# Kernel tuning notes

Hardware: AMD Instinct MI355X
Metric: run time of the kernel (lower is better)

The kernel has to match this reference:

```python
import jax, jax.numpy as jnp
import numpy as np

B, C, H, W = 64, 3, 224, 224
PH = PW = 16
GH, GW = H // PH, W // PW
NP = GH * GW                        # 196 patches
E = 512                             # embed_dim == decoder_dim
NH = 8                              # num_heads
PPD = C * PH * PW                   # 768 pixels per patch
MASK_RATIO = 0.75
NUM_MASKED = int(MASK_RATIO * NP)   # 147


def setup_inputs() -> dict:
    key = jax.random.key(0)
    ks = jax.random.split(key, 16)
    s = 0.02
    x = jax.random.normal(ks[0], (B, C, H, W), jnp.float32)
    # per-sample random permutation (torch.rand().argsort() equivalent)
    shuffle_indices = jax.vmap(lambda k: jax.random.permutation(k, NP))(
        jax.random.split(ks[1], B)).astype(jnp.int32)
    return {
        "x": x,
        "shuffle_indices": shuffle_indices,
        "W_pe": jax.random.normal(ks[2], (E, PPD), jnp.float32) * s,
        "b_pe": jnp.zeros((E,), jnp.float32),
        "pos_embed": jax.random.normal(ks[3], (1, NP, E), jnp.float32),
        "enc_W": jax.random.normal(ks[4], (E, E), jnp.float32) * s,
        "enc_b": jnp.zeros((E,), jnp.float32),
        "in_proj_w": jax.random.normal(ks[5], (3 * E, E), jnp.float32) * s,
        "in_proj_b": jnp.zeros((3 * E,), jnp.float32),
        "out_w": jax.random.normal(ks[6], (E, E), jnp.float32) * s,
        "out_b": jnp.zeros((E,), jnp.float32),
        "head_W": jax.random.normal(ks[7], (PPD, E), jnp.float32) * s,
        "head_b": jnp.zeros((PPD,), jnp.float32),
        # torch.randn_like(mask_patches) noise, passed in for determinism
        "noise": jax.random.normal(ks[8], (B, NUM_MASKED, PPD), jnp.float32),
    }


def _to_img(p):
    # [b, nP, ph*pw*c] -> [b, c, H, W] (inverse of patchify)
    return p.reshape(B, GH, GW, PH, PW, C).transpose(0, 5, 1, 3, 2, 4).reshape(B, C, H, W)


def reference(x, shuffle_indices, W_pe, b_pe, pos_embed, enc_W, enc_b,
              in_proj_w, in_proj_b, out_w, out_b, head_W, head_b, noise):
    hd = E // NH
    # patchify: [b,c,H,W] -> [b, nP, ph*pw*c]
    patches = x.reshape(B, C, GH, PH, GW, PW).transpose(0, 2, 4, 3, 5, 1).reshape(B, NP, PPD)

    mask_ind = shuffle_indices[:, :NUM_MASKED]      # [b, 147]
    unmask_ind = shuffle_indices[:, NUM_MASKED:]    # [b, 49]
    bi = jnp.arange(B)[:, None]
    mask_patches = patches[bi, mask_ind]            # [b,147,768]
    unmask_patches = patches[bi, unmask_ind]        # [b, 49,768]

    # mask_image: unmasked patches copied from x, masked patches = 1
    is_masked = jnp.zeros((B, NP), bool).at[bi, mask_ind].set(True)
    mpix = is_masked.reshape(B, 1, GH, 1, GW, 1)
    mpix = jnp.broadcast_to(mpix, (B, C, GH, PH, GW, PW)).reshape(B, C, H, W)
    mask_image = jnp.where(mpix, jnp.ones_like(x), x)

    # encode visible tokens
    pe = pos_embed[0]                               # [nP, E]
    unmask_tokens = unmask_patches @ W_pe.T + b_pe + pe[unmask_ind]
    encoded = jax.nn.gelu(unmask_tokens @ enc_W.T + enc_b)   # encoder.transformer stand-in

    # decode: cross attention (queries = mask tokens, kv = encoded)
    mask_tokens = mask_patches @ W_pe.T + b_pe + pe[mask_ind]
    Wq, Wk, Wv = jnp.split(in_proj_w, 3)
    bq, bk, bv = jnp.split(in_proj_b, 3)
    q = (mask_tokens @ Wq.T + bq).reshape(B, NUM_MASKED, NH, hd)
    k = (encoded @ Wk.T + bk).reshape(B, -1, NH, hd)
    v = (encoded @ Wv.T + bv).reshape(B, -1, NH, hd)
    attn = jax.nn.softmax(jnp.einsum('bqhd,bkhd->bhqk', q, k) / jnp.sqrt(jnp.float32(hd)), axis=-1)
    attn_out = jnp.einsum('bhqk,bkhd->bqhd', attn, v).reshape(B, NUM_MASKED, E) @ out_w.T + out_b

    # scatter encoded + attended tokens back into full sequence
    output_tokens = (jnp.zeros((B, NP, E), x.dtype)
                     .at[bi, unmask_ind].set(encoded)
                     .at[bi, mask_ind].set(attn_out))
    dec_mask_tokens = output_tokens[bi, mask_ind]
    pred = dec_mask_tokens @ head_W.T + head_b      # [b,147,768]

    mse_all_patches = jnp.abs(pred - mask_patches).mean(axis=-1).mean()

    recons_patches = jax.lax.stop_gradient(patches).at[bi, mask_ind].set(pred)
    recons_img = _to_img(recons_patches)

    patches_noisy = patches.at[bi, mask_ind].set(noise)
    patches_to_img = _to_img(patches_noisy)

    return recons_img, patches_to_img, mse_all_patches, mask_image
```

## Files before the change

### kernel.cpp

```cpp
#include <hip/hip_runtime.h>
#include <math.h>

typedef __attribute__((ext_vector_type(8))) __bf16 bf16x8;
typedef __attribute__((ext_vector_type(8))) unsigned short u16x8;
typedef __attribute__((ext_vector_type(4))) float f32x4;

typedef unsigned int as1_u32 __attribute__((address_space(1)));
typedef unsigned int as3_u32 __attribute__((address_space(3)));

__device__ __forceinline__ float bf2f(unsigned short h){
  return __uint_as_float(((unsigned int)h) << 16);
}
__device__ __forceinline__ unsigned short f2bf(float f){
  unsigned int u = __float_as_uint(f);
  unsigned int r = (u + 0x7FFFu + ((u >> 16) & 1u)) >> 16;
  return (unsigned short)r;
}

#if __has_builtin(__builtin_amdgcn_global_load_lds)
#define HAVE_GLOAD_LDS 1
__device__ __forceinline__ void gload16(const void* g, void* l){
  __builtin_amdgcn_global_load_lds((const as1_u32*)(unsigned long long)g,
                                   (as3_u32*)l, 16, 0, 0);
}
#else
#define HAVE_GLOAD_LDS 0
#endif

__global__ __launch_bounds__(256) void prep_all(
    const int* __restrict__ shuf, int* __restrict__ slot, int* __restrict__ invp,
    const float* __restrict__ Wpe, const float* __restrict__ outw,
    unsigned short* __restrict__ WpeT, unsigned short* __restrict__ outwT,
    const float* __restrict__ encW, const float* __restrict__ inW,
    const float* __restrict__ headW, unsigned short* __restrict__ wcat,
    const float* __restrict__ pos, const float* __restrict__ b_pe,
    const float* __restrict__ outb, const float* __restrict__ headb,
    unsigned short* __restrict__ pe2b, float* __restrict__ bh32)
{
  const int bid = blockIdx.x, t = threadIdx.x;
  __shared__ float tile[32][33];
  if (bid < 49){
    const int i = bid*256 + t;
    if (i < 64*196){
      const int b = i / 196, j = i % 196;
      const int p = shuf[b*196 + j];
      slot[b*196 + p] = (j < 147) ? j : -1;
      invp[b*196 + p] = j;
    }
  } else if (bid < 689){
    int b2 = bid - 49;
    const float* src; unsigned short* dst; int R, C, bx, by;
    if (b2 < 384){ src = Wpe;  dst = WpeT;  R = 512; C = 768; bx = b2 % 24; by = b2 / 24; }
    else { b2 -= 384; src = outw; dst = outwT; R = 512; C = 512; bx = b2 % 16; by = b2 / 16; }
    const int tx = t & 31, ty = t >> 5;
    #pragma unroll
    for (int i = 0; i < 4; i++)
      tile[ty + i*8][tx] = src[(size_t)(by*32 + ty + i*8)*C + bx*32 + tx];
    __syncthreads();
    #pragma unroll
    for (int i = 0; i < 4; i++)
      dst[(size_t)(bx*32 + ty + i*8)*R + by*32 + tx] = f2bf(tile[tx][ty + i*8]);
  } else if (bid < 6321){
    const int i = (bid - 689)*256 + t;
    float v;
    if      (i <  262144) v = encW[i];
    else if (i < 1048576) v = inW[i -  262144];
    else                  v = headW[i - 1048576];
    wcat[i] = f2bf(v);
  } else if (bid < 6833){
    const int i = (bid - 6321)*256 + t;
    pe2b[i] = (i < 100352) ? f2bf(pos[i] + b_pe[i & 511]) : (unsigned short)0;
  } else {
    const int r = (bid - 6833)*64 + (t >> 2);
    const int q4 = t & 3;
    float a = 0.0f;
    const float* hw = headW + (size_t)r*512 + q4*128;
    const float* ob = outb + q4*128;
    for (int e = 0; e < 128; e++) a += hw[e] * ob[e];
    a += __shfl_down(a, 2, 4);
    a += __shfl_down(a, 1, 4);
    if (q4 == 0) bh32[r] = a + headb[r];
  }
}

struct GD {
  const unsigned short* A; const unsigned short* W; const float* aux;
  const int* tok; unsigned short* ob; float* of;
  int N, K, mode, blk0, nx;
};

__device__ __forceinline__ void gemm_core(const GD g, int local, unsigned char* smem){
  const int tn = (local % g.nx) * 64;
  const int tm = (local / g.nx) * 128;
  const int N = g.N, K = g.K;
  unsigned short* As = (unsigned short*)smem;
  unsigned short* Bs = (unsigned short*)(smem + 2*128*32*2);
  const int t = threadIdx.x;
  const int wave = t >> 6, lane = t & 63;
  const int wr = (wave >> 1) * 64, wc = (wave & 1) * 32;
  const int lr = lane & 15, lg = lane >> 4;

  f32x4 acc[4][2] = {};
  const int nt = K >> 5;

#if HAVE_GLOAD_LDS
  const int srow = lane >> 2;
  const int scol = (lane & 3) * 8;
  const unsigned short* Ag = g.A + (size_t)(tm + wave*32 + srow) * K + scol;
  const unsigned short* Bg = g.W + (size_t)(tn + wave*16 + srow) * K + scol;
  const size_t rstepA = (size_t)16 * K;

  auto issue = [&](int tile_i, int slot_i){
    const int k0 = tile_i * 32;
    unsigned short* Al = As + slot_i*(128*32) + wave*(32*32);
    unsigned short* Bl = Bs + slot_i*(64*32)  + wave*(16*32);
    gload16(Ag + k0,          Al);
    gload16(Ag + k0 + rstepA, Al + 16*32);
    gload16(Bg + k0,          Bl);
  };

  issue(0, 0);
  __syncthreads();

  for (int tt = 0; tt < nt; ++tt){
    const int cur = tt & 1;
    if (tt + 1 < nt) issue(tt + 1, cur ^ 1);
    const unsigned short* Ab = As + cur*(128*32);
    const unsigned short* Bb = Bs + cur*(64*32);
    bf16x8 av[4], bv[2];
    #pragma unroll
    for (int mi = 0; mi < 4; mi++) av[mi] = *(const bf16x8*)&Ab[(wr + mi*16 + lr)*32 + lg*8];
    #pragma unroll
    for (int ni = 0; ni < 2; ni++) bv[ni] = *(const bf16x8*)&Bb[(wc + ni*16 + lr)*32 + lg*8];
    #pragma unroll
    for (int mi = 0; mi < 4; mi++)
      #pragma unroll
      for (int ni = 0; ni < 2; ni++)
        acc[mi][ni] = __builtin_amdgcn_mfma_f32_16x16x32_bf16(av[mi], bv[ni], acc[mi][ni], 0, 0, 0);
    __syncthreads();
  }
#else
  unsigned short* As1 = (unsigned short*)smem;
  unsigned short* Bs1 = (unsigned short*)(smem + 128*32*2);
  const int r0 = t >> 2;
  const int c0 = (t & 3) * 8;
  for (int k0 = 0; k0 < K; k0 += 32){
    u16x8 ra0 = *(const u16x8*)(g.A + (size_t)(tm + r0) * K + k0 + c0);
    u16x8 rb0 = (r0 < 64) ? *(const u16x8*)(g.W + (size_t)(tn + r0) * K + k0 + c0) : u16x8{};
    __syncthreads();
    *(u16x8*)&As1[r0 * 32 + c0] = ra0;
    if (r0 < 64) *(u16x8*)&Bs1[r0 * 32 + c0] = rb0;
    __syncthreads();
    bf16x8 av[4], bv[2];
    #pragma unroll
    for (int mi = 0; mi < 4; mi++) av[mi] = *(const bf16x8*)&As1[(wr + mi*16 + lr)*32 + lg*8];
    #pragma unroll
    for (int ni = 0; ni < 2; ni++) bv[ni] = *(const bf16x8*)&Bs1[(wc + ni*16 + lr)*32 + lg*8];
    #pragma unroll
    for (int mi = 0; mi < 4; mi++)
      #pragma unroll
      for (int ni = 0; ni < 2; ni++)
        acc[mi][ni] = __builtin_amdgcn_mfma_f32_16x16x32_bf16(av[mi], bv[ni], acc[mi][ni], 0, 0, 0);
  }
#endif

  const int mode = g.mode;
  #pragma unroll
  for (int ni = 0; ni < 2; ni++){
    const int gcol = tn + wc + ni*16 + lr;
    const float bval = (mode == 0 || mode == 3) ? g.aux[gcol] : 0.0f;
    #pragma unroll
    for (int mi = 0; mi < 4; mi++){
      #pragma unroll
      for (int jj = 0; jj < 4; jj++){
        const int grow = tm + wr + mi*16 + lg*4 + jj;
        float v = acc[mi][ni][jj] + bval;
        if (mode == 1 || mode == 2) v += g.aux[(size_t)(g.tok[grow] & 255) * 512 + gcol];
        if (mode == 2){
          const float u = v;
          v = 0.5f * u * (1.0f + tanhf(0.7978845608f * (u + 0.044715f * u * u * u)));
        }
        if (mode == 3) g.of[(size_t)grow * N + gcol] = v;
        else           g.ob[(size_t)grow * N + gcol] = f2bf(v);
      }
    }
  }
}

__global__ __launch_bounds__(256) void gemm_one(GD g){
  __shared__ __align__(16) unsigned char smem[24576];
  gemm_core(g, blockIdx.x, smem);
}
__global__ __launch_bounds__(256) void gemm_two(GD a, GD b){
  __shared__ __align__(16) unsigned char smem[24576];
  GD g = (blockIdx.x >= b.blk0) ? b : a;
  gemm_core(g, blockIdx.x - g.blk0, smem);
}

__global__ __launch_bounds__(256) void fold_patch(GD g0, GD g1, GD g2, GD g3, GD g4,
    const float* __restrict__ x, const int* __restrict__ invp,
    unsigned short* __restrict__ maskA, unsigned short* __restrict__ unmaskA,
    int* __restrict__ tokcat)
{
  __shared__ __align__(16) unsigned char smem[24576];
  const int bid = blockIdx.x, t = threadIdx.x;
  if (bid < 176){
    GD g = g0;
    if (bid >= g1.blk0) g = g1;
    if (bid >= g2.blk0) g = g2;
    if (bid >= g3.blk0) g = g3;
    if (bid >= g4.blk0) g = g4;
    gemm_core(g, bid - g.blk0, smem);
    return;
  }
  const int blk = bid - 176;
  const int b = blk / 14, gh = blk % 14;
  unsigned short* ld = (unsigned short*)smem;
  for (int e = t; e < 2688; e += 256){
    const int w4 = e % 56, rest = e / 56;
    const int phi = rest & 15, c = rest >> 4;
    const f32x4 v4 = *(const f32x4*)(x + (size_t)b*150528 + c*50176
                                     + (size_t)(gh*16 + phi)*224 + w4*4);
    const int gw = w4 >> 2, part = w4 & 3;
    const int dbase = gw*768 + phi*48 + part*12 + c;
    ld[dbase]     = f2bf(v4[0]);
    ld[dbase + 3] = f2bf(v4[1]);
    ld[dbase + 6] = f2bf(v4[2]);
    ld[dbase + 9] = f2bf(v4[3]);
  }
  __syncthreads();
  for (int e = t; e < 1344; e += 256){
    const int gw = e / 96, elem8 = e % 96;
    const int p = gh*14 + gw;
    const int j = invp[b*196 + p];
    unsigned short* dst;
    int row;
    if (j < 147){ row = b*160 + j;        dst = maskA; }
    else        { row = b*64 + (j - 147); dst = unmaskA; }
    *(u16x8*)&dst[(size_t)row*768 + elem8*8] = *(const u16x8*)&ld[gw*768 + elem8*8];
    if (elem8 == 0) tokcat[(j < 147) ? (b*160 + j) : (10240 + b*64 + (j - 147))] = p;
  }
}

__global__ __launch_bounds__(256) void attn_mfma(const unsigned short* __restrict__ qb,
                                                 const unsigned short* __restrict__ kv,
                                                 unsigned short* __restrict__ attnout)
{
  __shared__ __align__(16) unsigned char smem[72064];
  unsigned short* qs  = (unsigned short*)smem;
  unsigned short* ks  = (unsigned short*)(smem + 27648);
  unsigned short* vsT = (unsigned short*)(smem + 36864);
  unsigned short* pwt = (unsigned short*)(smem + 46080);
  float* inv_ = (float*)(smem + 71424);
  const int b = blockIdx.x >> 3, h = blockIdx.x & 7;
  const int t = threadIdx.x;
  const int wave = t >> 6, lane = t & 63;
  const int wr = (wave >> 1) * 96, wc = (wave & 1) * 32;
  const int lr = lane & 15, lg = lane >> 4;

  for (int idx = t; idx < 192*8; idx += 256){
    const int i = idx >> 3, g = idx & 7;
    u16x8 v = {};
    if (i < 160) v = *(const u16x8*)(qb + (size_t)(b*160 + i)*512 + h*64 + g*8);
    *(u16x8*)&qs[i*72 + g*8] = v;
  }
  for (int idx = t; idx < 64*8; idx += 256){
    const int j = idx >> 3, g = idx & 7;
    const size_t base = (size_t)(b*64 + j)*1024 + h*64 + g*8;
    u16x8 k8 = *(const u16x8*)(kv + base);
    u16x8 v8 = *(const u16x8*)(kv + base + 512);
    *(u16x8*)&ks[j*72 + g*8] = k8;
    #pragma unroll
    for (int d = 0; d < 8; d++) vsT[(g*8 + d)*72 + j] = v8[d];
  }
  __syncthreads();

  {
    f32x4 acc[6][2] = {};
    #pragma unroll
    for (int ksv = 0; ksv < 2; ksv++){
      const int kk = ksv*32;
      bf16x8 av[6], bv[2];
      #pragma unroll
      for (int mi = 0; mi < 6; mi++) av[mi] = *(const bf16x8*)&qs[(wr + mi*16 + lr)*72 + kk + lg*8];
      #pragma unroll
      for (int ni = 0; ni < 2; ni++) bv[ni] = *(const bf16x8*)&ks[(wc + ni*16 + lr)*72 + kk + lg*8];
      #pragma unroll
      for (int mi = 0; mi < 6; mi++)
        #pragma unroll
        for (int ni = 0; ni < 2; ni++)
          acc[mi][ni] = __builtin_amdgcn_mfma_f32_16x16x32_bf16(av[mi], bv[ni], acc[mi][ni], 0, 0, 0);
    }
    #pragma unroll
    for (int mi = 0; mi < 6; mi++)
      #pragma unroll
      for (int ni = 0; ni < 2; ni++)
        #pragma unroll
        for (int jj = 0; jj < 4; jj++)
          pwt[(wr + mi*16 + lg*4 + jj)*66 + wc + ni*16 + lr] = f2bf(acc[mi][ni][jj] * 0.125f);
  }
  __syncthreads();

  unsigned short* pa = qs;
  if (t < 147){
    float sc[49];
    float m = -1e30f;
    #pragma unroll 7
    for (int j = 0; j < 49; j++){ sc[j] = bf2f(pwt[t*66 + j]); m = fmaxf(m, sc[j]); }
    float sum = 0.0f;
    for (int j = 0; j < 49; j++){
      const float e = __expf(sc[j] - m);
      sum += e;
      pa[t*72 + j] = f2bf(e);
    }
    inv_[t] = 1.0f / sum;
    for (int j = 49; j < 64; j++) pa[t*72 + j] = 0;
  } else if (t < 192){
    for (int j = 0; j < 64; j++) pa[t*72 + j] = 0;
    if (t < 160) inv_[t] = 0.0f;
  }
  __syncthreads();

  {
    f32x4 acc[6][2] = {};
    #pragma unroll
    for (int ksv = 0; ksv < 2; ksv++){
      const int kk = ksv*32;
      bf16x8 av[6], bv[2];
      #pragma unroll
      for (int mi = 0; mi < 6; mi++) av[mi] = *(const bf16x8*)&pa[(wr + mi*16 + lr)*72 + kk + lg*8];
      #pragma unroll
      for (int ni = 0; ni < 2; ni++) bv[ni] = *(const bf16x8*)&vsT[(wc + ni*16 + lr)*72 + kk + lg*8];
      #pragma unroll
      for (int mi = 0; mi < 6; mi++)
        #pragma unroll
        for (int ni = 0; ni < 2; ni++)
          acc[mi][ni] = __builtin_amdgcn_mfma_f32_16x16x32_bf16(av[mi], bv[ni], acc[mi][ni], 0, 0, 0);
    }
    #pragma unroll
    for (int mi = 0; mi < 6; mi++)
      #pragma unroll
      for (int ni = 0; ni < 2; ni++)
        #pragma unroll
        for (int jj = 0; jj < 4; jj++){
          const int grow = wr + mi*16 + lg*4 + jj;
          if (grow < 160){
            const float v = acc[mi][ni][jj] * inv_[grow];
            attnout[(size_t)(b*160 + grow)*512 + h*64 + wc + ni*16 + lr] = f2bf(v);
          }
        }
  }
}

__global__ __launch_bounds__(256) void finalize_k(const float* __restrict__ x, const int* __restrict__ slot,
                           const unsigned short* __restrict__ predb, const float* __restrict__ noise,
                           float* __restrict__ out, float* __restrict__ partial)
{
  const int i4 = blockIdx.x * 256 + threadIdx.x;
  const int idx = i4 * 4;
  const int w = idx % 224;
  const int h = (idx / 224) % 224;
  const int c = (idx / 50176) % 3;
  const int b = idx / 150528;
  const f32x4 xv = *(const f32x4*)(x + idx);
  const int p = (h >> 4) * 14 + (w >> 4);
  const int s = slot[b*196 + p];
  f32x4 rec = xv, noi = xv, mim = xv;
  float a = 0.0f;
  if (s >= 0){
    const int d = (h & 15)*48 + (w & 15)*3 + c;
    const size_t pb = (size_t)(b*160 + s)*768 + d;
    const size_t nb = (size_t)(b*147 + s)*768 + d;
    rec = f32x4{bf2f(predb[pb]), bf2f(predb[pb+3]), bf2f(predb[pb+6]), bf2f(predb[pb+9])};
    noi = f32x4{noise[nb], noise[nb+3], noise[nb+6], noise[nb+9]};
    mim = f32x4{1.0f, 1.0f, 1.0f, 1.0f};
    a = fabsf(rec[0] - xv[0]) + fabsf(rec[1] - xv[1]) + fabsf(rec[2] - xv[2]) + fabsf(rec[3] - xv[3]);
  }
  *(f32x4*)(out + idx) = rec;
  *(f32x4*)(out + 9633792 + idx) = noi;
  float prevm = __shfl_up(mim[3], 1);
  if ((threadIdx.x & 63) == 0 && idx > 0){
    const int pidx = idx - 1;
    const int pw2 = pidx % 224, ph2 = (pidx / 224) % 224;
    const int pb2 = pidx / 150528;
    const int pp = (ph2 >> 4) * 14 + (pw2 >> 4);
    prevm = (slot[pb2*196 + pp] >= 0) ? 1.0f : x[pidx];
  }
  *(f32x4*)(out + 19267584 + idx) = f32x4{prevm, mim[0], mim[1], mim[2]};
  if (i4 == 2408447) out[28901376] = mim[3];
  #pragma unroll
  for (int o = 32; o > 0; o >>= 1) a += __shfl_down(a, o);
  __shared__ float wsum[4];
  if ((threadIdx.x & 63) == 0) wsum[threadIdx.x >> 6] = a;
  __syncthreads();
  if (threadIdx.x == 0)
    partial[blockIdx.x] = wsum[0] + wsum[1] + wsum[2] + wsum[3];
}

__global__ __launch_bounds__(1024) void mse_reduce(const float* __restrict__ partial, float* __restrict__ out){
  float a = 0.0f;
  for (int i = threadIdx.x; i < 9408; i += 1024) a += partial[i];
  #pragma unroll
  for (int o = 32; o > 0; o >>= 1) a += __shfl_down(a, o);
  __shared__ float wsum[16];
  if ((threadIdx.x & 63) == 0) wsum[threadIdx.x >> 6] = a;
  __syncthreads();
  if (threadIdx.x == 0){
    float s = 0.0f;
    #pragma unroll
    for (int i = 0; i < 16; i++) s += wsum[i];
    out[19267584] = s * (1.0f / 7225344.0f);
  }
}

extern "C" void kernel_launch(void* const* d_in, const int* in_sizes, int n_in,
                              void* d_out, int out_size, void* d_ws, size_t ws_size,
                              hipStream_t stream)
{
  const float* x     = (const float*)d_in[0];
  const int*   shuf  = (const int*)d_in[1];
  const float* W_pe  = (const float*)d_in[2];
  const float* b_pe  = (const float*)d_in[3];
  const float* pos   = (const float*)d_in[4];
  const float* encW  = (const float*)d_in[5];
  const float* encB  = (const float*)d_in[6];
  const float* inW   = (const float*)d_in[7];
  const float* inB   = (const float*)d_in[8];
  const float* outW  = (const float*)d_in[9];
  const float* outB  = (const float*)d_in[10];
  const float* headW = (const float*)d_in[11];
  const float* headB = (const float*)d_in[12];
  const float* noise = (const float*)d_in[13];
  float* out = (float*)d_out;

  char* ws = (char*)d_ws;
  size_t cur = 0;
  auto alloc = [&](size_t bytes){ size_t o = cur; cur += (bytes + 255) & ~(size_t)255; return o; };

  int*   slot    = (int*)(ws + alloc(64*196*4));
  int*   invp    = (int*)(ws + alloc(64*196*4));
  int*   tokcat  = (int*)(ws + alloc(14336*4));
  float* partial = (float*)(ws + alloc(9408*4));
  unsigned short* wcat    = (unsigned short*)(ws + alloc((size_t)1441792*2));
  unsigned short* encw_b  = wcat;
  unsigned short* inw_b   = wcat +  262144;
  unsigned short* headw_b = wcat + 1048576;
  unsigned short* WpeT  = (unsigned short*)(ws + alloc((size_t)393216*2));
  unsigned short* outwT = (unsigned short*)(ws + alloc((size_t)262144*2));
  unsigned short* Wqpe  = (unsigned short*)(ws + alloc((size_t)393216*2));
  unsigned short* Wepe  = (unsigned short*)(ws + alloc((size_t)393216*2));
  unsigned short* Whp   = (unsigned short*)(ws + alloc((size_t)393216*2));
  unsigned short* pe2b  = (unsigned short*)(ws + alloc((size_t)131072*2));
  float* peq  = (float*)(ws + alloc((size_t)131072*4));
  float* pee  = (float*)(ws + alloc((size_t)131072*4));
  float* bh32 = (float*)(ws + alloc(768*4));
  char* R0 = ws + alloc(26214400);
  unsigned short* maskA   = (unsigned short*)R0;
  unsigned short* unmaskA = (unsigned short*)(R0 + 15728640);
  unsigned short* attnout = (unsigned short*)R0;
  unsigned short* predb   = (unsigned short*)(R0 + 10485760);
  unsigned short* enc   = (unsigned short*)(ws + alloc((size_t)2097152*2));
  unsigned short* qb    = (unsigned short*)(ws + alloc((size_t)5242880*2));
  unsigned short* kvb   = (unsigned short*)(ws + alloc((size_t)4194304*2));

  prep_all<<<6845, 256, 0, stream>>>(shuf, slot, invp, W_pe, outW, WpeT, outwT,
                                     encW, inW, headW, wcat,
                                     pos, b_pe, outB, headB, pe2b, bh32);

  {
    GD t1 = { inw_b,  WpeT,   nullptr, nullptr, Wqpe,   nullptr, 768, 512, 4,   0, 12 };
    GD t2 = { encw_b, WpeT,   nullptr, nullptr, Wepe,   nullptr, 768, 512, 4,  48, 12 };
    GD t3 = { headw_b,outwT,  nullptr, nullptr, Whp,    nullptr, 512, 512, 4,  96,  8 };
    GD t4 = { pe2b,   inw_b,  inB,     nullptr, nullptr, peq,    512, 512, 3, 144,  8 };
    GD t5 = { pe2b,   encw_b, encB,    nullptr, nullptr, pee,    512, 512, 3, 160,  8 };
    fold_patch<<<1072, 256, 0, stream>>>(t1, t2, t3, t4, t5, x, invp, maskA, unmaskA, tokcat);
  }
  {
    GD q  = { maskA,   Wqpe, peq, tokcat,         qb,  nullptr, 512, 768, 1,   0, 8 };
    GD en = { unmaskA, Wepe, pee, tokcat + 10240, enc, nullptr, 512, 768, 2, 640, 8 };
    gemm_two<<<896, 256, 0, stream>>>(q, en);
  }
  {
    GD kv = { enc, inw_b + (size_t)512*512, inB + 512, nullptr, kvb, nullptr, 1024, 512, 0, 0, 16 };
    gemm_one<<<512, 256, 0, stream>>>(kv);
  }
  attn_mfma<<<512, 256, 0, stream>>>(qb, kvb, attnout);
  {
    GD pr = { attnout, Whp, bh32, nullptr, predb, nullptr, 768, 512, 0, 0, 12 };
    gemm_one<<<960, 256, 0, stream>>>(pr);
  }

  finalize_k<<<9408, 256, 0, stream>>>(x, slot, predb, noise, out, partial);
  mse_reduce<<<1, 1024, 0, stream>>>(partial, out);
}
```

Measured before the change: 178.2 us.

## Restructure finalize kernel to process patch rows with vectorized contiguous loads

The finalize kernel now maps each thread to 4 pixels of one patch row across all 3 channels. This lets it read prediction, noise and masked-patch data as contiguous vector loads instead of strided scalar gathers, and masked patches skip the x read. The MSE is now computed against the bf16 patch copy in maskA instead of fp32 x, so maskA and predb get separate workspace buffers rather than aliased ones. The grid shrinks by 3x, and the partial-sum buffer and reduction shrink to match.

```diff
diff --git a/kernel.cpp b/kernel.cpp
--- a/kernel.cpp
+++ b/kernel.cpp
@@ -3,6 +3,7 @@
 
 typedef __attribute__((ext_vector_type(8))) __bf16 bf16x8;
 typedef __attribute__((ext_vector_type(8))) unsigned short u16x8;
+typedef __attribute__((ext_vector_type(4))) unsigned short u16x4;
 typedef __attribute__((ext_vector_type(4))) float f32x4;
 
 typedef unsigned int as1_u32 __attribute__((address_space(1)));
@@ -353,41 +354,67 @@
 }
 
 __global__ __launch_bounds__(256) void finalize_k(const float* __restrict__ x, const int* __restrict__ slot,
-                           const unsigned short* __restrict__ predb, const float* __restrict__ noise,
+                           const unsigned short* __restrict__ predb, const unsigned short* __restrict__ maskA,
+                           const float* __restrict__ noise,
                            float* __restrict__ out, float* __restrict__ partial)
 {
-  const int i4 = blockIdx.x * 256 + threadIdx.x;
-  const int idx = i4 * 4;
-  const int w = idx % 224;
-  const int h = (idx / 224) % 224;
-  const int c = (idx / 50176) % 3;
-  const int b = idx / 150528;
-  const f32x4 xv = *(const f32x4*)(x + idx);
-  const int p = (h >> 4) * 14 + (w >> 4);
+  const int tg = blockIdx.x * 256 + threadIdx.x;
+  const int part = tg & 3, phi = (tg >> 2) & 15;
+  const int pp = tg >> 6;
+  const int b = pp / 196, p = pp % 196;
+  const int gh = p / 14, gw = p % 14;
   const int s = slot[b*196 + p];
-  f32x4 rec = xv, noi = xv, mim = xv;
+  const int h = gh*16 + phi, w0 = gw*16 + part*4;
+  const int rowbase = b*150528 + h*224 + w0;
+  const int d0 = phi*48 + part*12;
+  f32x4 rec[3], noi[3], mim[3];
   float a = 0.0f;
   if (s >= 0){
-    const int d = (h & 15)*48 + (w & 15)*3 + c;
-    const size_t pb = (size_t)(b*160 + s)*768 + d;
-    const size_t nb = (size_t)(b*147 + s)*768 + d;
-    rec = f32x4{bf2f(predb[pb]), bf2f(predb[pb+3]), bf2f(predb[pb+6]), bf2f(predb[pb+9])};
-    noi = f32x4{noise[nb], noise[nb+3], noise[nb+6], noise[nb+9]};
-    mim = f32x4{1.0f, 1.0f, 1.0f, 1.0f};
-    a = fabsf(rec[0] - xv[0]) + fabsf(rec[1] - xv[1]) + fabsf(rec[2] - xv[2]) + fabsf(rec[3] - xv[3]);
-  }
-  *(f32x4*)(out + idx) = rec;
-  *(f32x4*)(out + 9633792 + idx) = noi;
-  float prevm = __shfl_up(mim[3], 1);
-  if ((threadIdx.x & 63) == 0 && idx > 0){
-    const int pidx = idx - 1;
-    const int pw2 = pidx % 224, ph2 = (pidx / 224) % 224;
-    const int pb2 = pidx / 150528;
-    const int pp = (ph2 >> 4) * 14 + (pw2 >> 4);
-    prevm = (slot[pb2*196 + pp] >= 0) ? 1.0f : x[pidx];
-  }
-  *(f32x4*)(out + 19267584 + idx) = f32x4{prevm, mim[0], mim[1], mim[2]};
-  if (i4 == 2408447) out[28901376] = mim[3];
+    const size_t pb = (size_t)(b*160 + s)*768 + d0;
+    const size_t nb = (size_t)(b*147 + s)*768 + d0;
+    u16x4 p0 = *(const u16x4*)(predb + pb), p1 = *(const u16x4*)(predb + pb + 4), p2 = *(const u16x4*)(predb + pb + 8);
+    u16x4 m0 = *(const u16x4*)(maskA + pb), m1 = *(const u16x4*)(maskA + pb + 4), m2 = *(const u16x4*)(maskA + pb + 8);
+    f32x4 n0 = *(const f32x4*)(noise + nb), n1 = *(const f32x4*)(noise + nb + 4), n2 = *(const f32x4*)(noise + nb + 8);
+    float pr[12], mk[12], nz[12];
+    #pragma unroll
+    for (int e = 0; e < 4; e++){
+      pr[e] = bf2f(p0[e]); pr[4+e] = bf2f(p1[e]); pr[8+e] = bf2f(p2[e]);
+      mk[e] = bf2f(m0[e]); mk[4+e] = bf2f(m1[e]); mk[8+e] = bf2f(m2[e]);
+      nz[e] = n0[e];       nz[4+e] = n1[e];       nz[8+e] = n2[e];
+    }
+    #pragma unroll
+    for (int e = 0; e < 12; e++) a += fabsf(pr[e] - mk[e]);
+    #pragma unroll
+    for (int c = 0; c < 3; c++){
+      rec[c] = f32x4{pr[c], pr[3+c], pr[6+c], pr[9+c]};
+      noi[c] = f32x4{nz[c], nz[3+c], nz[6+c], nz[9+c]};
+      mim[c] = f32x4{1.0f, 1.0f, 1.0f, 1.0f};
+    }
+  } else {
+    #pragma unroll
+    for (int c = 0; c < 3; c++){
+      const f32x4 xv = *(const f32x4*)(x + rowbase + c*50176);
+      rec[c] = xv; noi[c] = xv; mim[c] = xv;
+    }
+  }
+  #pragma unroll
+  for (int c = 0; c < 3; c++){
+    const int gbase = rowbase + c*50176;
+    *(f32x4*)(out + gbase) = rec[c];
+    *(f32x4*)(out + 9633792 + gbase) = noi[c];
+    float prevm = __shfl_up(mim[c][3], 1);
+    if (part == 0){
+      const int pidx = gbase - 1;
+      if (pidx >= 0){
+        const int w2 = pidx % 224, h2 = (pidx / 224) % 224;
+        const int b2 = pidx / 150528;
+        const int p2i = (h2 >> 4) * 14 + (w2 >> 4);
+        prevm = (slot[b2*196 + p2i] >= 0) ? 1.0f : x[pidx];
+      } else prevm = 0.0f;
+    }
+    *(f32x4*)(out + 19267584 + gbase) = f32x4{prevm, mim[c][0], mim[c][1], mim[c][2]};
+  }
+  if (tg == 802815) out[28901376] = mim[2][3];
   #pragma unroll
   for (int o = 32; o > 0; o >>= 1) a += __shfl_down(a, o);
   __shared__ float wsum[4];
@@ -399,7 +426,7 @@
 
 __global__ __launch_bounds__(1024) void mse_reduce(const float* __restrict__ partial, float* __restrict__ out){
   float a = 0.0f;
-  for (int i = threadIdx.x; i < 9408; i += 1024) a += partial[i];
+  for (int i = threadIdx.x; i < 3136; i += 1024) a += partial[i];
   #pragma unroll
   for (int o = 32; o > 0; o >>= 1) a += __shfl_down(a, o);
   __shared__ float wsum[16];
@@ -440,7 +467,7 @@
   int*   slot    = (int*)(ws + alloc(64*196*4));
   int*   invp    = (int*)(ws + alloc(64*196*4));
   int*   tokcat  = (int*)(ws + alloc(14336*4));
-  float* partial = (float*)(ws + alloc(9408*4));
+  float* partial = (float*)(ws + alloc(3136*4));
   unsigned short* wcat    = (unsigned short*)(ws + alloc((size_t)1441792*2));
   unsigned short* encw_b  = wcat;
   unsigned short* inw_b   = wcat +  262144;
@@ -454,11 +481,10 @@
   float* peq  = (float*)(ws + alloc((size_t)131072*4));
   float* pee  = (float*)(ws + alloc((size_t)131072*4));
   float* bh32 = (float*)(ws + alloc(768*4));
-  char* R0 = ws + alloc(26214400);
-  unsigned short* maskA   = (unsigned short*)R0;
-  unsigned short* unmaskA = (unsigned short*)(R0 + 15728640);
-  unsigned short* attnout = (unsigned short*)R0;
-  unsigned short* predb   = (unsigned short*)(R0 + 10485760);
+  unsigned short* maskA   = (unsigned short*)(ws + alloc((size_t)7864320*2));
+  unsigned short* unmaskA = (unsigned short*)(ws + alloc((size_t)3145728*2));
+  unsigned short* attnout = (unsigned short*)(ws + alloc((size_t)5242880*2));
+  unsigned short* predb   = (unsigned short*)(ws + alloc((size_t)7864320*2));
   unsigned short* enc   = (unsigned short*)(ws + alloc((size_t)2097152*2));
   unsigned short* qb    = (unsigned short*)(ws + alloc((size_t)5242880*2));
   unsigned short* kvb   = (unsigned short*)(ws + alloc((size_t)4194304*2));
@@ -490,6 +516,6 @@
     gemm_one<<<960, 256, 0, stream>>>(pr);
   }
 
-  finalize_k<<<9408, 256, 0, stream>>>(x, slot, predb, noise, out, partial);
+  finalize_k<<<3136, 256, 0, stream>>>(x, slot, predb, maskA, noise, out, partial);
   mse_reduce<<<1, 1024, 0, stream>>>(partial, out);
 }
```

Result: slower. 181.9 us (+2.1%).

## Fuse MSE reduction into finalize via last-block atomic and vectorize weight casts

Applied to the files above, without the earlier changes.

Removes the separate single-block mse_reduce launch: each finalize block bumps a global counter, and the last block to arrive sums all partials and writes the mean. A counter reset is added to prep_all. The fp32-to-bf16 weight cast and pos-embed prep loops now handle four elements per thread, which cuts the prep grid size. The aliased R0 workspace region is also split into separate buffers. The cost is an atomic plus fence in every finalize block and a serialized tail reduction inside the last block.

```diff
diff --git a/kernel.cpp b/kernel.cpp
--- a/kernel.cpp
+++ b/kernel.cpp
@@ -3,6 +3,7 @@
 
 typedef __attribute__((ext_vector_type(8))) __bf16 bf16x8;
 typedef __attribute__((ext_vector_type(8))) unsigned short u16x8;
+typedef __attribute__((ext_vector_type(4))) unsigned short u16x4;
 typedef __attribute__((ext_vector_type(4))) float f32x4;
 
 typedef unsigned int as1_u32 __attribute__((address_space(1)));
@@ -29,6 +30,7 @@
 
 __global__ __launch_bounds__(256) void prep_all(
     const int* __restrict__ shuf, int* __restrict__ slot, int* __restrict__ invp,
+    int* __restrict__ ctr,
     const float* __restrict__ Wpe, const float* __restrict__ outw,
     unsigned short* __restrict__ WpeT, unsigned short* __restrict__ outwT,
     const float* __restrict__ encW, const float* __restrict__ inW,
@@ -40,6 +42,7 @@
   const int bid = blockIdx.x, t = threadIdx.x;
   __shared__ float tile[32][33];
   if (bid < 49){
+    if (bid == 0 && t == 0) ctr[0] = 0;
     const int i = bid*256 + t;
     if (i < 64*196){
       const int b = i / 196, j = i % 196;
@@ -60,18 +63,25 @@
     #pragma unroll
     for (int i = 0; i < 4; i++)
       dst[(size_t)(bx*32 + ty + i*8)*R + by*32 + tx] = f2bf(tile[tx][ty + i*8]);
-  } else if (bid < 6321){
-    const int i = (bid - 689)*256 + t;
-    float v;
-    if      (i <  262144) v = encW[i];
-    else if (i < 1048576) v = inW[i -  262144];
-    else                  v = headW[i - 1048576];
-    wcat[i] = f2bf(v);
-  } else if (bid < 6833){
-    const int i = (bid - 6321)*256 + t;
-    pe2b[i] = (i < 100352) ? f2bf(pos[i] + b_pe[i & 511]) : (unsigned short)0;
+  } else if (bid < 2097){
+    const int i = ((bid - 689)*256 + t) * 4;
+    f32x4 v;
+    if      (i <  262144) v = *(const f32x4*)(encW + i);
+    else if (i < 1048576) v = *(const f32x4*)(inW + (i - 262144));
+    else                  v = *(const f32x4*)(headW + (i - 1048576));
+    u16x4 o = { f2bf(v[0]), f2bf(v[1]), f2bf(v[2]), f2bf(v[3]) };
+    *(u16x4*)(wcat + i) = o;
+  } else if (bid < 2225){
+    const int i = ((bid - 2097)*256 + t) * 4;
+    u16x4 o = {0, 0, 0, 0};
+    if (i < 100352){
+      const f32x4 pv = *(const f32x4*)(pos + i);
+      const f32x4 bv = *(const f32x4*)(b_pe + (i & 511));
+      o = u16x4{ f2bf(pv[0]+bv[0]), f2bf(pv[1]+bv[1]), f2bf(pv[2]+bv[2]), f2bf(pv[3]+bv[3]) };
+    }
+    *(u16x4*)(pe2b + i) = o;
   } else {
-    const int r = (bid - 6833)*64 + (t >> 2);
+    const int r = (bid - 2225)*64 + (t >> 2);
     const int q4 = t & 3;
     float a = 0.0f;
     const float* hw = headW + (size_t)r*512 + q4*128;
@@ -354,7 +364,7 @@
 
 __global__ __launch_bounds__(256) void finalize_k(const float* __restrict__ x, const int* __restrict__ slot,
                            const unsigned short* __restrict__ predb, const float* __restrict__ noise,
-                           float* __restrict__ out, float* __restrict__ partial)
+                           float* __restrict__ out, float* __restrict__ partial, int* __restrict__ ctr)
 {
   const int i4 = blockIdx.x * 256 + threadIdx.x;
   const int idx = i4 * 4;
@@ -391,25 +401,25 @@
   #pragma unroll
   for (int o = 32; o > 0; o >>= 1) a += __shfl_down(a, o);
   __shared__ float wsum[4];
+  __shared__ int isLast;
   if ((threadIdx.x & 63) == 0) wsum[threadIdx.x >> 6] = a;
   __syncthreads();
-  if (threadIdx.x == 0)
+  if (threadIdx.x == 0){
     partial[blockIdx.x] = wsum[0] + wsum[1] + wsum[2] + wsum[3];
-}
-
-__global__ __launch_bounds__(1024) void mse_reduce(const float* __restrict__ partial, float* __restrict__ out){
-  float a = 0.0f;
-  for (int i = threadIdx.x; i < 9408; i += 1024) a += partial[i];
-  #pragma unroll
-  for (int o = 32; o > 0; o >>= 1) a += __shfl_down(a, o);
-  __shared__ float wsum[16];
-  if ((threadIdx.x & 63) == 0) wsum[threadIdx.x >> 6] = a;
-  __syncthreads();
-  if (threadIdx.x == 0){
-    float s = 0.0f;
-    #pragma unroll
-    for (int i = 0; i < 16; i++) s += wsum[i];
-    out[19267584] = s * (1.0f / 7225344.0f);
+    __threadfence();
+    isLast = (atomicAdd(ctr, 1) == 9407);
+  }
+  __syncthreads();
+  if (isLast){
+    __threadfence();
+    float s2 = 0.0f;
+    for (int i = threadIdx.x; i < 9408; i += 256) s2 += partial[i];
+    #pragma unroll
+    for (int o = 32; o > 0; o >>= 1) s2 += __shfl_down(s2, o);
+    if ((threadIdx.x & 63) == 0) wsum[threadIdx.x >> 6] = s2;
+    __syncthreads();
+    if (threadIdx.x == 0)
+      out[19267584] = (wsum[0] + wsum[1] + wsum[2] + wsum[3]) * (1.0f / 7225344.0f);
   }
 }
 
@@ -440,6 +450,7 @@
   int*   slot    = (int*)(ws + alloc(64*196*4));
   int*   invp    = (int*)(ws + alloc(64*196*4));
   int*   tokcat  = (int*)(ws + alloc(14336*4));
+  int*   ctr     = (int*)(ws + alloc(256));
   float* partial = (float*)(ws + alloc(9408*4));
   unsigned short* wcat    = (unsigned short*)(ws + alloc((size_t)1441792*2));
   unsigned short* encw_b  = wcat;
@@ -454,16 +465,15 @@
   float* peq  = (float*)(ws + alloc((size_t)131072*4));
   float* pee  = (float*)(ws + alloc((size_t)131072*4));
   float* bh32 = (float*)(ws + alloc(768*4));
-  char* R0 = ws + alloc(26214400);
-  unsigned short* maskA   = (unsigned short*)R0;
-  unsigned short* unmaskA = (unsigned short*)(R0 + 15728640);
-  unsigned short* attnout = (unsigned short*)R0;
-  unsigned short* predb   = (unsigned short*)(R0 + 10485760);
+  unsigned short* maskA   = (unsigned short*)(ws + alloc((size_t)7864320*2));
+  unsigned short* unmaskA = (unsigned short*)(ws + alloc((size_t)3145728*2));
+  unsigned short* attnout = (unsigned short*)(ws + alloc((size_t)5242880*2));
+  unsigned short* predb   = (unsigned short*)(ws + alloc((size_t)7864320*2));
   unsigned short* enc   = (unsigned short*)(ws + alloc((size_t)2097152*2));
   unsigned short* qb    = (unsigned short*)(ws + alloc((size_t)5242880*2));
   unsigned short* kvb   = (unsigned short*)(ws + alloc((size_t)4194304*2));
 
-  prep_all<<<6845, 256, 0, stream>>>(shuf, slot, invp, W_pe, outW, WpeT, outwT,
+  prep_all<<<2237, 256, 0, stream>>>(shuf, slot, invp, ctr, W_pe, outW, WpeT, outwT,
                                      encW, inW, headW, wcat,
                                      pos, b_pe, outB, headB, pe2b, bh32);
 
@@ -490,6 +500,5 @@
     gemm_one<<<960, 256, 0, stream>>>(pr);
   }
 
-  finalize_k<<<9408, 256, 0, stream>>>(x, slot, predb, noise, out, partial);
-  mse_reduce<<<1, 1024, 0, stream>>>(partial, out);
-}
+  finalize_k<<<9408, 256, 0, stream>>>(x, slot, predb, noise, out, partial, ctr);
+}
```

After: 516.2 us. +189.7%, slower.
